# Performance work log

Hardware: AMD Instinct MI355X
Metric: run time of the kernel (lower is better)

Reference implementation:

```python
import jax, jax.numpy as jnp
import numpy as np

# Grid / model constants (from cfg: scene_bbox [0,0,0,102.4,102.4,6.4], featmap_size=quant_size=0.4, n_input=5, batch=2)
B, N = 2, 300000
X, Y, Z, T = 256, 256, 16, 5
QUANT = np.array([0.4, 0.4, 0.4, 1.0], dtype=np.float32)
C_MID, N_CLASSES = 8, 1  # MinkUNet14 INIT_DIM=8, out=n_classes=1
KOFF = 3  # 3^4 = 81 kernel offsets of the first 4D sparse conv


def setup_inputs() -> dict:
    key = jax.random.key(0)
    ks = jax.random.split(key, 5)
    xyz = jax.random.uniform(ks[0], (B, N, 3), dtype=jnp.float32) * jnp.array([102.4, 102.4, 6.4], jnp.float32)
    t = jax.random.randint(ks[1], (B, N, 1), 0, T).astype(jnp.float32)
    points = jnp.concatenate([xyz, t], axis=-1)  # [B, N, 4] 4D point clouds (x,y,z,t)
    W0 = jax.random.normal(ks[2], (KOFF**4, 1, C_MID), jnp.float32) * 0.1  # per-offset GEMM weights
    b0 = jnp.zeros((C_MID,), jnp.float32)
    W1 = jax.random.normal(ks[3], (C_MID, N_CLASSES), jnp.float32) * 0.1  # pointwise head
    b1 = jnp.zeros((N_CLASSES,), jnp.float32)
    return {"points": points, "W0": W0, "b0": b0, "W1": W1, "b1": b1}


def _voxelize(points):
    """Quantize 4D points and unweighted-average per-voxel features (ME.TensorField.sparse())."""
    coords = jnp.floor(points / jnp.asarray(QUANT)).astype(jnp.int32)  # [B, N, 4]
    cx = jnp.clip(coords[..., 0], 0, X - 1)
    cy = jnp.clip(coords[..., 1], 0, Y - 1)
    cz = jnp.clip(coords[..., 2], 0, Z - 1)
    ct = jnp.clip(coords[..., 3], 0, T - 1)
    lin = ((cx * Y + cy) * Z + cz) * T + ct            # [B, N] linear voxel index
    lin = (lin + jnp.arange(B, dtype=jnp.int32)[:, None] * (X * Y * Z * T)).reshape(-1)
    feats = jnp.full((B * N,), 0.5, points.dtype)      # feats = 0.5 * ones(len(pcd), 1)
    nseg = B * X * Y * Z * T
    s = jax.ops.segment_sum(feats, lin, num_segments=nseg)
    cnt = jax.ops.segment_sum(jnp.ones_like(feats), lin, num_segments=nseg)
    occ = cnt > 0
    avg = jnp.where(occ, s / jnp.maximum(cnt, 1.0), 0.0)
    grid = avg.reshape(B, X, Y, Z, T, 1)               # densified sparse features (zeros at empty voxels)
    mask = occ.reshape(B, X, Y, Z, T, 1).astype(points.dtype)
    return grid, mask


def reference(points, W0, b0, W1, b1):
    grid, mask = _voxelize(points)
    # 4D generalized sparse conv (kernel 3^4), stride 1: out coords == in coords.
    # Densified form: shift-gather neighbors, GEMM with per-offset weights, accumulate, mask to occupied voxels.
    pad = jnp.pad(grid, ((0, 0), (1, 1), (1, 1), (1, 1), (1, 1), (0, 0)))
    out = jnp.zeros(grid.shape[:-1] + (C_MID,), grid.dtype)
    k = 0
    for dx in range(KOFF):
        for dy in range(KOFF):
            for dz in range(KOFF):
                for dt in range(KOFF):
                    nb = pad[:, dx:dx + X, dy:dy + Y, dz:dz + Z, dt:dt + T, :]  # [B,X,Y,Z,T,1]
                    out = out + nb @ W0[k]
                    k += 1
    out = jax.nn.relu((out + b0) * mask)
    out = (out @ W1 + b1) * mask                        # pointwise sparse conv to n_classes
    return jnp.moveaxis(out, -1, 1)                     # dense featmap [B, 1, X, Y, Z, T]
```

## Files before the change

### kernel.cpp

```cpp
#include <hip/hip_runtime.h>

#define XD 256
#define YD 256
#define ZD 16
#define TD 5
#define BD 2
#define NP 300000
#define CMID 8
#define VPB (XD * YD * ZD * TD)
#define NVOX (BD * VPB)
#define MAXPTS (BD * NP)

#define OCC8_BYTES (BD * XD * YD * ZD * 8)
#define OCC8_U128  (OCC8_BYTES / 16)
#define NCOL   (BD * XD * YD)
#define PK_BYTES (NCOL * 16)

#define SCAT_BLOCKS ((MAXPTS + 255) / 256)
#define CONV_BLOCKS 2048
#define STRIP 5120
#define QCAP 512

__global__ __launch_bounds__(256) void zero_kernel(uint4* __restrict__ occ) {
    int i = blockIdx.x * 256 + threadIdx.x;
    uint4 z = {0u, 0u, 0u, 0u};
    for (int j = i; j < OCC8_U128; j += 2048 * 256) occ[j] = z;
}

__global__ __launch_bounds__(256) void scatter_kernel(
    const float4* __restrict__ pts, unsigned char* __restrict__ occ8) {
    int i = blockIdx.x * 256 + threadIdx.x;
    if (i >= MAXPTS) return;
    float4 p = pts[i];
    int cx = min(max((int)floorf(p.x / 0.4f), 0), XD - 1);
    int cy = min(max((int)floorf(p.y / 0.4f), 0), YD - 1);
    int cz = min(max((int)floorf(p.z / 0.4f), 0), ZD - 1);
    int ct = min(max((int)floorf(p.w / 1.0f), 0), TD - 1);
    int b  = i / NP;
    unsigned a = (((unsigned)b << 23) | ((unsigned)cx << 15) |
                  ((unsigned)cy << 7) | ((unsigned)cz << 3) | (unsigned)ct);
    occ8[a] = 1;
}

__device__ __forceinline__ unsigned pack8(unsigned long long v) {
    v |= v >> 7;
    v |= v >> 14;
    v |= v >> 28;
    return (unsigned)v & 0xffu;
}

__global__ __launch_bounds__(256) void pack_kernel(
    const ulonglong2* __restrict__ occ16, unsigned short* __restrict__ pk) {
    int j = blockIdx.x * 256 + threadIdx.x;
    ulonglong2 v = occ16[j];
    pk[j] = (unsigned short)(pack8(v.x) | (pack8(v.y) << 8));
}

__global__ __launch_bounds__(256) void conv_kernel(
    const ulonglong2* __restrict__ pk128,
    const float* __restrict__ W0,
    const float* __restrict__ b0,
    const float* __restrict__ W1,
    const float* __restrict__ b1,
    float4* __restrict__ out4) {
    __shared__ float tab[216 * 12];
    __shared__ unsigned long long clo[3 * 66];
    __shared__ unsigned long long chi[3 * 66];
    __shared__ unsigned short queue[QCAP];
    __shared__ float outt[STRIP];
    __shared__ unsigned wsum[4];
    __shared__ float b0s[CMID];
    __shared__ float w1s[CMID];
    __shared__ float b1sv;

    int tid = threadIdx.x;
    int s   = blockIdx.x;
    int b   = s >> 10;
    int x   = (s >> 2) & 255;
    int ny0 = (s & 3) << 6;

    float4* ot4 = (float4*)outt;
    float4 zf = {0.f, 0.f, 0.f, 0.f};
#pragma unroll
    for (int j = 0; j < 5; ++j) ot4[tid + j * 256] = zf;

    if (tid < 216) {
        int kb = tid >> 3;
        int m  = tid & 7;
        float acc[CMID];
#pragma unroll
        for (int c = 0; c < CMID; ++c) acc[c] = 0.0f;
#pragma unroll
        for (int dti = 0; dti < 3; ++dti) {
            if ((m >> dti) & 1) {
                const float* w = &W0[(kb * 3 + dti) * CMID];
#pragma unroll
                for (int c = 0; c < CMID; ++c) acc[c] += w[c];
            }
        }
#pragma unroll
        for (int c = 0; c < CMID; ++c) tab[tid * 12 + c] = acc[c];
    }
    if (tid < CMID) {
        b0s[tid] = b0[tid];
        w1s[tid] = W1[tid];
    }
    if (tid == 0) b1sv = b1[0];

    if (tid < 3 * 66) {
        int r   = tid / 66;
        int cyl = tid % 66;
        int nx  = x + r - 1;
        int cy  = ny0 + cyl - 1;
        bool valid = ((unsigned)nx < XD) && ((unsigned)cy < YD);
        ulonglong2 v = pk128[(b << 16) | ((nx & 255) << 8) | (cy & 255)];
        clo[tid] = valid ? v.x : 0ull;
        chi[tid] = valid ? v.y : 0ull;
    }
    __syncthreads();

    {
    }
    unsigned long long cw = (tid & 2) ? chi[67 + (tid >> 2)]
                                      : clo[67 + (tid >> 2)];
    unsigned w = (unsigned)((tid & 1) ? (cw >> 32) : cw);
    int cnt = __popc(w);

    unsigned pre = (unsigned)cnt;
#pragma unroll
    for (int off = 1; off < 64; off <<= 1) {
        unsigned v = (unsigned)__shfl_up((int)pre, off, 64);
        if ((tid & 63) >= off) pre += v;
    }
    int wv = tid >> 6;
    if ((tid & 63) == 63) wsum[wv] = pre;
    __syncthreads();
    unsigned base = 0;
#pragma unroll
    for (int k = 0; k < 4; ++k) base += (k < wv) ? wsum[k] : 0u;
    unsigned qlen = wsum[0] + wsum[1] + wsum[2] + wsum[3];
    if (qlen > QCAP) qlen = QCAP;
    unsigned pos  = base + pre - (unsigned)cnt;

    {
        int cl = tid >> 2;
        int zb = (tid & 3) << 2;
        unsigned ww = w;
        while (ww) {
            int bi = __ffs(ww) - 1;
            ww &= ww - 1;
            int zz = zb + (bi >> 3);
            int tt = bi & 7;
            if (pos < QCAP)
                queue[pos] = (unsigned short)((cl << 7) | (zz << 3) | tt);
            ++pos;
        }
    }
    __syncthreads();

    for (unsigned q = tid; q < qlen; q += 256) {
        int e  = queue[q];
        int cl = e >> 7;
        int z  = (e >> 3) & 15;
        int t  = e & 7;

        unsigned mask27 = 0u;
        unsigned long long mpA = 0ull, mpB = 0ull;
#pragma unroll
        for (int dxi = 0; dxi < 3; ++dxi) {
#pragma unroll
            for (int dyi = 0; dyi < 3; ++dyi) {
                int ci = dxi * 66 + cl + dyi;
                unsigned long long lo = clo[ci];
                unsigned long long hi = chi[ci];
                int k0 = (dxi * 3 + dyi) * 3;
#pragma unroll
                for (int dzi = 0; dzi < 3; ++dzi) {
                    int k = k0 + dzi;
                    int nz = z + dzi - 1;
                    unsigned sh = ((unsigned)nz * 8u) & 63u;
                    unsigned r = (unsigned)(((nz & 8) ? (hi >> sh)
                                                      : (lo >> sh)) & 0xffull);
                    r = ((unsigned)nz < ZD) ? r : 0u;
                    unsigned m = ((r << 1) >> t) & 7u;
                    mask27 |= (m ? 1u : 0u) << k;
                    if (k < 21) mpA |= (unsigned long long)m << (3 * k);
                    else        mpB |= (unsigned long long)m << (3 * (k - 21));
                }
            }
        }

        float4 h0 = zf, h1 = zf;
        while (mask27) {
            int k = __ffs(mask27) - 1;
            mask27 &= mask27 - 1;
            unsigned long long mp = (k < 21) ? mpA : mpB;
            int kk = (k < 21) ? k : k - 21;
            unsigned m = (unsigned)(mp >> (3 * kk)) & 7u;
            const float4* row = (const float4*)&tab[(k * 8 + (int)m) * 12];
            h0 += row[0];
            h1 += row[1];
        }

        float hc[CMID] = {h0.x, h0.y, h0.z, h0.w, h1.x, h1.y, h1.z, h1.w};
        float o = 0.0f;
#pragma unroll
        for (int c = 0; c < CMID; ++c) {
            float v = 0.5f * hc[c] + b0s[c];
            v = v > 0.0f ? v : 0.0f;
            o += v * w1s[c];
        }
        outt[cl * 80 + z * 5 + t] = o + b1sv;
    }
    __syncthreads();

    const float4* src = (const float4*)outt;
    float4* dst = out4 + ((size_t)b * (VPB / 4)) + (size_t)(x * YD + ny0) * 20;
#pragma unroll
    for (int j = 0; j < 5; ++j) dst[tid + j * 256] = src[tid + j * 256];
}

extern "C" void kernel_launch(void* const* d_in, const int* in_sizes, int n_in,
                              void* d_out, int out_size, void* d_ws, size_t ws_size,
                              hipStream_t stream) {
    const float4* pts = (const float4*)d_in[0];
    const float* W0   = (const float*)d_in[1];
    const float* b0   = (const float*)d_in[2];
    const float* W1   = (const float*)d_in[3];
    const float* b1   = (const float*)d_in[4];
    unsigned char* occ8 = (unsigned char*)d_ws;
    unsigned short* pk  = (unsigned short*)((char*)d_ws + OCC8_BYTES);

    zero_kernel<<<2048, 256, 0, stream>>>((uint4*)occ8);
    scatter_kernel<<<SCAT_BLOCKS, 256, 0, stream>>>(pts, occ8);
    pack_kernel<<<OCC8_U128 / 256, 256, 0, stream>>>(
        (const ulonglong2*)occ8, pk);
    conv_kernel<<<CONV_BLOCKS, 256, 0, stream>>>(
        (const ulonglong2*)pk, W0, b0, W1, b1, (float4*)d_out);
}
```

Baseline: 45.67 us.

## Halve conv strip size and gather neighbor masks with direct 81-bit mask bitwalk

The conv kernel now processes 32 y-columns per block with 128 threads across 4096 blocks, which shrinks halo and shared memory per block and raises block count. The neighbor-mask construction extracts a 24-bit z-window per (dx,dy) column with one funnel shift and packs nine bits directly into an 81-bit mask. It accumulates raw W0 rows per set bit instead of using the precomputed 216-entry t-combination table. This removes the table build and per-k decoding, but may do up to three times as many row accumulations per voxel and repeats the halo loads more often.

```diff
diff --git a/kernel.cpp b/kernel.cpp
--- a/kernel.cpp
+++ b/kernel.cpp
@@ -14,11 +14,10 @@
 #define OCC8_BYTES (BD * XD * YD * ZD * 8)
 #define OCC8_U128  (OCC8_BYTES / 16)
 #define NCOL   (BD * XD * YD)
-#define PK_BYTES (NCOL * 16)
 
 #define SCAT_BLOCKS ((MAXPTS + 255) / 256)
-#define CONV_BLOCKS 2048
-#define STRIP 5120
+#define CONV_BLOCKS 4096
+#define CTHR 128
 #define QCAP 512
 
 __global__ __launch_bounds__(256) void zero_kernel(uint4* __restrict__ occ) {
@@ -56,50 +55,37 @@
     pk[j] = (unsigned short)(pack8(v.x) | (pack8(v.y) << 8));
 }
 
-__global__ __launch_bounds__(256) void conv_kernel(
+__global__ __launch_bounds__(CTHR) void conv_kernel(
     const ulonglong2* __restrict__ pk128,
     const float* __restrict__ W0,
     const float* __restrict__ b0,
     const float* __restrict__ W1,
     const float* __restrict__ b1,
     float4* __restrict__ out4) {
-    __shared__ float tab[216 * 12];
-    __shared__ unsigned long long clo[3 * 66];
-    __shared__ unsigned long long chi[3 * 66];
+    __shared__ float w0s[81 * 12];
+    __shared__ unsigned long long clo[3 * 34];
+    __shared__ unsigned long long chi[3 * 34];
     __shared__ unsigned short queue[QCAP];
-    __shared__ float outt[STRIP];
-    __shared__ unsigned wsum[4];
+    __shared__ float outt[32 * 80];
+    __shared__ unsigned wsum[2];
     __shared__ float b0s[CMID];
     __shared__ float w1s[CMID];
     __shared__ float b1sv;
 
     int tid = threadIdx.x;
     int s   = blockIdx.x;
-    int b   = s >> 10;
-    int x   = (s >> 2) & 255;
-    int ny0 = (s & 3) << 6;
+    int b   = s >> 11;
+    int x   = (s >> 3) & 255;
+    int ny0 = (s & 7) << 5;
 
     float4* ot4 = (float4*)outt;
     float4 zf = {0.f, 0.f, 0.f, 0.f};
 #pragma unroll
-    for (int j = 0; j < 5; ++j) ot4[tid + j * 256] = zf;
-
-    if (tid < 216) {
-        int kb = tid >> 3;
-        int m  = tid & 7;
-        float acc[CMID];
-#pragma unroll
-        for (int c = 0; c < CMID; ++c) acc[c] = 0.0f;
-#pragma unroll
-        for (int dti = 0; dti < 3; ++dti) {
-            if ((m >> dti) & 1) {
-                const float* w = &W0[(kb * 3 + dti) * CMID];
-#pragma unroll
-                for (int c = 0; c < CMID; ++c) acc[c] += w[c];
-            }
-        }
-#pragma unroll
-        for (int c = 0; c < CMID; ++c) tab[tid * 12 + c] = acc[c];
+    for (int j = 0; j < 5; ++j) ot4[tid + j * CTHR] = zf;
+
+    if (tid < 81) {
+#pragma unroll
+        for (int c = 0; c < CMID; ++c) w0s[tid * 12 + c] = W0[tid * CMID + c];
     }
     if (tid < CMID) {
         b0s[tid] = b0[tid];
@@ -107,9 +93,9 @@
     }
     if (tid == 0) b1sv = b1[0];
 
-    if (tid < 3 * 66) {
-        int r   = tid / 66;
-        int cyl = tid % 66;
+    if (tid < 3 * 34) {
+        int r   = tid / 34;
+        int cyl = tid % 34;
         int nx  = x + r - 1;
         int cy  = ny0 + cyl - 1;
         bool valid = ((unsigned)nx < XD) && ((unsigned)cy < YD);
@@ -119,10 +105,8 @@
     }
     __syncthreads();
 
-    {
-    }
-    unsigned long long cw = (tid & 2) ? chi[67 + (tid >> 2)]
-                                      : clo[67 + (tid >> 2)];
+    unsigned long long cw = (tid & 2) ? chi[35 + (tid >> 2)]
+                                      : clo[35 + (tid >> 2)];
     unsigned w = (unsigned)((tid & 1) ? (cw >> 32) : cw);
     int cnt = __popc(w);
 
@@ -135,12 +119,9 @@
     int wv = tid >> 6;
     if ((tid & 63) == 63) wsum[wv] = pre;
     __syncthreads();
-    unsigned base = 0;
-#pragma unroll
-    for (int k = 0; k < 4; ++k) base += (k < wv) ? wsum[k] : 0u;
-    unsigned qlen = wsum[0] + wsum[1] + wsum[2] + wsum[3];
+    unsigned qlen = wsum[0] + wsum[1];
     if (qlen > QCAP) qlen = QCAP;
-    unsigned pos  = base + pre - (unsigned)cnt;
+    unsigned pos = ((wv == 1) ? wsum[0] : 0u) + pre - (unsigned)cnt;
 
     {
         int cl = tid >> 2;
@@ -158,46 +139,48 @@
     }
     __syncthreads();
 
-    for (unsigned q = tid; q < qlen; q += 256) {
+    for (unsigned q = tid; q < qlen; q += CTHR) {
         int e  = queue[q];
         int cl = e >> 7;
         int z  = (e >> 3) & 15;
         int t  = e & 7;
 
-        unsigned mask27 = 0u;
-        unsigned long long mpA = 0ull, mpB = 0ull;
+        unsigned long long mpA = 0ull;
+        unsigned mpB = 0u;
+        int sft = (z - 1) * 8;
 #pragma unroll
         for (int dxi = 0; dxi < 3; ++dxi) {
 #pragma unroll
             for (int dyi = 0; dyi < 3; ++dyi) {
-                int ci = dxi * 66 + cl + dyi;
+                int ci = dxi * 34 + cl + dyi;
                 unsigned long long lo = clo[ci];
                 unsigned long long hi = chi[ci];
-                int k0 = (dxi * 3 + dyi) * 3;
-#pragma unroll
-                for (int dzi = 0; dzi < 3; ++dzi) {
-                    int k = k0 + dzi;
-                    int nz = z + dzi - 1;
-                    unsigned sh = ((unsigned)nz * 8u) & 63u;
-                    unsigned r = (unsigned)(((nz & 8) ? (hi >> sh)
-                                                      : (lo >> sh)) & 0xffull);
-                    r = ((unsigned)nz < ZD) ? r : 0u;
-                    unsigned m = ((r << 1) >> t) & 7u;
-                    mask27 |= (m ? 1u : 0u) << k;
-                    if (k < 21) mpA |= (unsigned long long)m << (3 * k);
-                    else        mpB |= (unsigned long long)m << (3 * (k - 21));
-                }
+                unsigned long long wv64 =
+                    (z == 0) ? (lo << 8)
+                  : (z <= 8) ? ((lo >> sft) | ((hi << 1) << (63 - sft)))
+                             : (hi >> (sft - 64));
+                unsigned qw = (((unsigned)wv64 & 0xffffffu) << 1) >> t;
+                unsigned nine = (qw & 7u) | (((qw >> 8) & 7u) << 3) |
+                                (((qw >> 16) & 7u) << 6);
+                int c9 = dxi * 3 + dyi;
+                if (c9 < 7) mpA |= (unsigned long long)nine << (9 * c9);
+                else if (c9 == 7) mpB |= nine;
+                else mpB |= nine << 9;
             }
         }
 
         float4 h0 = zf, h1 = zf;
-        while (mask27) {
-            int k = __ffs(mask27) - 1;
-            mask27 &= mask27 - 1;
-            unsigned long long mp = (k < 21) ? mpA : mpB;
-            int kk = (k < 21) ? k : k - 21;
-            unsigned m = (unsigned)(mp >> (3 * kk)) & 7u;
-            const float4* row = (const float4*)&tab[(k * 8 + (int)m) * 12];
+        while (mpA) {
+            int j = __ffsll((unsigned long long)mpA) - 1;
+            mpA &= mpA - 1;
+            const float4* row = (const float4*)&w0s[j * 12];
+            h0 += row[0];
+            h1 += row[1];
+        }
+        while (mpB) {
+            int j = __ffs(mpB) - 1;
+            mpB &= mpB - 1;
+            const float4* row = (const float4*)&w0s[(63 + j) * 12];
             h0 += row[0];
             h1 += row[1];
         }
@@ -217,7 +200,7 @@
     const float4* src = (const float4*)outt;
     float4* dst = out4 + ((size_t)b * (VPB / 4)) + (size_t)(x * YD + ny0) * 20;
 #pragma unroll
-    for (int j = 0; j < 5; ++j) dst[tid + j * 256] = src[tid + j * 256];
+    for (int j = 0; j < 5; ++j) dst[tid + j * CTHR] = src[tid + j * CTHR];
 }
 
 extern "C" void kernel_launch(void* const* d_in, const int* in_sizes, int n_in,
@@ -235,6 +218,6 @@
     scatter_kernel<<<SCAT_BLOCKS, 256, 0, stream>>>(pts, occ8);
     pack_kernel<<<OCC8_U128 / 256, 256, 0, stream>>>(
         (const ulonglong2*)occ8, pk);
-    conv_kernel<<<CONV_BLOCKS, 256, 0, stream>>>(
+    conv_kernel<<<CONV_BLOCKS, 128, 0, stream>>>(
         (const ulonglong2*)pk, W0, b0, W1, b1, (float4*)d_out);
 }
```

After: 42.88 us. 1.06x faster.
